# Optimization experiments

Hardware: AMD Instinct MI355X
Metric: run time of the kernel (lower is better)

Reference implementation:

```python
import jax, jax.numpy as jnp
import numpy as np


def setup_inputs() -> dict:
    key = jax.random.key(0)
    k1, k2 = jax.random.split(key)
    pred = jax.random.normal(k1, (1, 2048, 512), dtype=jnp.float32)
    cand = jax.random.normal(k2, (1, 65536, 512), dtype=jnp.float32)
    return {
        "predicted_transaction_company": pred,
        "future_transaction_companies_inc_current_data": cand,
    }


def reference(predicted_transaction_company, future_transaction_companies_inc_current_data):
    # torch.cdist with p=2 on [1,P,D] x [1,R,D] -> [1,P,R]; squeeze(0) -> [P,R]; global min.
    x = predicted_transaction_company[0]                       # [P, D]
    y = future_transaction_companies_inc_current_data[0]       # [R, D]
    sq = (
        jnp.sum(x * x, axis=-1)[:, None]
        + jnp.sum(y * y, axis=-1)[None, :]
        - 2.0 * jnp.einsum("pd,rd->pr", x, y)
    )                                                          # [P, R]
    distances = jnp.sqrt(jnp.maximum(sq, 0.0))
    return jnp.min(distances)
```

## Files before the change

### kernel.cpp

```cpp
#include <hip/hip_runtime.h>
#include <stdint.h>

#define P 2048
#define R 65536
#define DD 512
#define BT 128
#define BK 32

typedef __attribute__((ext_vector_type(8))) short short8;
typedef __attribute__((ext_vector_type(4))) float f32x4;

__device__ inline unsigned short f2bf(float f) {
  unsigned int u = __float_as_uint(f);
  u += 0x7fffu + ((u >> 16) & 1u);
  return (unsigned short)(u >> 16);
}

__device__ inline void gload_lds16(const void* g, void* l) {
  __builtin_amdgcn_global_load_lds(
      (const __attribute__((address_space(1))) unsigned int*)g,
      (__attribute__((address_space(3))) unsigned int*)l,
      16, 0, 0);
}

__global__ __launch_bounds__(256) void k_convert(
    const float* __restrict__ pred, const float* __restrict__ cand,
    unsigned short* __restrict__ Abf, unsigned short* __restrict__ Bbf,
    float* __restrict__ nx, float* __restrict__ ny,
    unsigned int* __restrict__ minp)
{
  if (blockIdx.x == 0 && threadIdx.x == 0) *minp = 0x7f800000u;
  int gw   = (blockIdx.x * 256 + threadIdx.x) >> 6;
  int lane = threadIdx.x & 63;
  if (gw >= P + R) return;
  const float* src; unsigned short* dst; float* np;
  if (gw < P) { src = pred + (size_t)gw * DD; dst = Abf + (size_t)gw * DD; np = nx + gw; }
  else { int r = gw - P; src = cand + (size_t)r * DD; dst = Bbf + (size_t)r * DD; np = ny + r; }
  const float4* s4 = ((const float4*)src) + lane * 2;
  float4 v0 = s4[0], v1 = s4[1];
  float ss = v0.x*v0.x + v0.y*v0.y + v0.z*v0.z + v0.w*v0.w
           + v1.x*v1.x + v1.y*v1.y + v1.z*v1.z + v1.w*v1.w;
  union { unsigned short h[8]; uint4 v; } pk;
  pk.h[0]=f2bf(v0.x); pk.h[1]=f2bf(v0.y); pk.h[2]=f2bf(v0.z); pk.h[3]=f2bf(v0.w);
  pk.h[4]=f2bf(v1.x); pk.h[5]=f2bf(v1.y); pk.h[6]=f2bf(v1.z); pk.h[7]=f2bf(v1.w);
  *(uint4*)(dst + (size_t)lane * 8) = pk.v;
  #pragma unroll
  for (int off = 32; off; off >>= 1) ss += __shfl_down(ss, off, 64);
  if (lane == 0) *np = ss;
}

__global__ __launch_bounds__(256) void k_gemm_min(
    const unsigned short* __restrict__ Abf, const unsigned short* __restrict__ Bbf,
    const float* __restrict__ nx, const float* __restrict__ ny,
    unsigned int* __restrict__ minp)
{
  __shared__ __align__(16) unsigned short As[BT * BK];
  __shared__ __align__(16) unsigned short Bs[BT * BK];
  __shared__ float wmin[4];

  const int tid  = threadIdx.x;
  const int wave = tid >> 6;
  const int lane = tid & 63;
  const int by = blockIdx.x & 15;
  const int bx = blockIdx.x >> 4;
  const int rowA0 = by * BT, rowB0 = bx * BT;
  const int wr = wave >> 1, wc = wave & 1;

  f32x4 zero = {0.f, 0.f, 0.f, 0.f};
  f32x4 acc[4][4];
  #pragma unroll
  for (int i = 0; i < 4; ++i)
    #pragma unroll
    for (int j = 0; j < 4; ++j) acc[i][j] = zero;

  const int t0 = wave * 2;
  const int r0 = t0 * 16 + (lane >> 2);
  const int cs = (lane & 3) * 8;
  const unsigned short* gA0 = Abf + (size_t)(rowA0 + r0) * DD + cs;
  const unsigned short* gA1 = Abf + (size_t)(rowA0 + r0 + 16) * DD + cs;
  const unsigned short* gB0 = Bbf + (size_t)(rowB0 + r0) * DD + cs;
  const unsigned short* gB1 = Bbf + (size_t)(rowB0 + r0 + 16) * DD + cs;
  unsigned short* lA0 = As + t0 * 512;
  unsigned short* lA1 = As + t0 * 512 + 512;
  unsigned short* lB0 = Bs + t0 * 512;
  unsigned short* lB1 = Bs + t0 * 512 + 512;

  const unsigned short* ap = As + ((wr * 64) + (lane & 15)) * BK + ((lane >> 4) * 8);
  const unsigned short* bp = Bs + ((wc * 64) + (lane & 15)) * BK + ((lane >> 4) * 8);

  for (int k0 = 0; k0 < DD; k0 += BK) {
    gload_lds16(gA0 + k0, lA0);
    gload_lds16(gA1 + k0, lA1);
    gload_lds16(gB0 + k0, lB0);
    gload_lds16(gB1 + k0, lB1);
    __syncthreads();

    short8 af[4], bfr[4];
    #pragma unroll
    for (int i = 0; i < 4; ++i) af[i]  = *(const short8*)(ap + i * 16 * BK);
    #pragma unroll
    for (int j = 0; j < 4; ++j) bfr[j] = *(const short8*)(bp + j * 16 * BK);
    #pragma unroll
    for (int i = 0; i < 4; ++i)
      #pragma unroll
      for (int j = 0; j < 4; ++j)
        acc[i][j] = __builtin_amdgcn_mfma_f32_16x16x32_bf16(af[i], bfr[j], acc[i][j], 0, 0, 0);
    __syncthreads();
  }

  const int quad = lane >> 4, n16 = lane & 15;
  float lmin = 3.4e38f;
  #pragma unroll
  for (int i = 0; i < 4; ++i) {
    const int mbase = rowA0 + wr * 64 + i * 16 + quad * 4;
    float4 nxv = *(const float4*)(nx + mbase);
    #pragma unroll
    for (int j = 0; j < 4; ++j) {
      const int n = rowB0 + wc * 64 + j * 16 + n16;
      const float nyv = ny[n];
      f32x4 a = acc[i][j];
      lmin = fminf(lmin, nxv.x + nyv - 2.0f * a[0]);
      lmin = fminf(lmin, nxv.y + nyv - 2.0f * a[1]);
      lmin = fminf(lmin, nxv.z + nyv - 2.0f * a[2]);
      lmin = fminf(lmin, nxv.w + nyv - 2.0f * a[3]);
    }
  }
  #pragma unroll
  for (int off = 32; off; off >>= 1) lmin = fminf(lmin, __shfl_down(lmin, off, 64));
  if (lane == 0) wmin[wave] = lmin;
  __syncthreads();
  if (tid == 0) {
    float m = fminf(fminf(wmin[0], wmin[1]), fminf(wmin[2], wmin[3]));
    atomicMin(minp, __float_as_uint(fmaxf(m, 0.0f)));
  }
}

__global__ __launch_bounds__(64) void k_initmin(unsigned int* minp) {
  if (threadIdx.x == 0) *minp = 0x7f800000u;
}

__global__ __launch_bounds__(256) void k_brute(
    const float* __restrict__ pred, const float* __restrict__ cand,
    unsigned int* __restrict__ minp)
{
  __shared__ float yrow[DD];
  __shared__ float wm[4];
  const int c = blockIdx.x;
  for (int i = threadIdx.x; i < DD; i += 256) yrow[i] = cand[(size_t)c * DD + i];
  __syncthreads();
  float lmin = 3.4e38f;
  for (int p = threadIdx.x; p < P; p += 256) {
    const float* xp = pred + (size_t)p * DD;
    float s = 0.f;
    for (int k = 0; k < DD; ++k) { float d = xp[k] - yrow[k]; s = fmaf(d, d, s); }
    lmin = fminf(lmin, s);
  }
  #pragma unroll
  for (int off = 32; off; off >>= 1) lmin = fminf(lmin, __shfl_down(lmin, off, 64));
  if ((threadIdx.x & 63) == 0) wm[threadIdx.x >> 6] = lmin;
  __syncthreads();
  if (threadIdx.x == 0) {
    float m = fminf(fminf(wm[0], wm[1]), fminf(wm[2], wm[3]));
    atomicMin(minp, __float_as_uint(fmaxf(m, 0.0f)));
  }
}

__global__ __launch_bounds__(64) void k_finalize(const unsigned int* minp, float* out) {
  if (threadIdx.x == 0) out[0] = sqrtf(__uint_as_float(*minp));
}

extern "C" void kernel_launch(void* const* d_in, const int* in_sizes, int n_in,
                              void* d_out, int out_size, void* d_ws, size_t ws_size,
                              hipStream_t stream) {
  const float* pred = (const float*)d_in[0];
  const float* cand = (const float*)d_in[1];
  float* out = (float*)d_out;

  unsigned int* minp = (unsigned int*)d_ws;
  float* wsf = (float*)d_ws;
  float* nx = wsf + 16;
  float* ny = nx + P;
  unsigned short* Abf = (unsigned short*)(ny + R);
  unsigned short* Bbf = Abf + (size_t)P * DD;
  const size_t need = (size_t)(16 + P + R) * 4 + ((size_t)P * DD + (size_t)R * DD) * 2;

  if (ws_size >= need) {
    const int rows = P + R;
    k_convert<<<rows / 4, 256, 0, stream>>>(pred, cand, Abf, Bbf, nx, ny, minp);
    k_gemm_min<<<(P / BT) * (R / BT), 256, 0, stream>>>(Abf, Bbf, nx, ny, minp);
  } else {
    k_initmin<<<1, 64, 0, stream>>>(minp);
    k_brute<<<R, 256, 0, stream>>>(pred, cand, minp);
  }
  k_finalize<<<1, 64, 0, stream>>>(minp, out);
}
```

Baseline: 402.6 us.

## Double K-tile depth to 64 and XOR-swizzle LDS layout for bank conflicts

Raises the K step of the bf16 MFMA GEMM tile from 32 to 64, so each barrier pair covers two MFMA rounds and the number of loop iterations and syncs is halved. The global-to-LDS loads are remapped to 8 rows per 16-byte-chunk group, with the column chunk XOR-swizzled by row, and the fragment reads apply the matching swizzle to avoid LDS bank conflicts on the 128-byte row stride. LDS use doubles to 32 KB per block, which may reduce occupancy, and there is still no double buffering.

```diff
diff --git a/kernel.cpp b/kernel.cpp
--- a/kernel.cpp
+++ b/kernel.cpp
@@ -5,7 +5,7 @@
 #define R 65536
 #define DD 512
 #define BT 128
-#define BK 32
+#define BK 64
 
 typedef __attribute__((ext_vector_type(8))) short short8;
 typedef __attribute__((ext_vector_type(4))) float f32x4;
@@ -73,33 +73,47 @@
     #pragma unroll
     for (int j = 0; j < 4; ++j) acc[i][j] = zero;
 
-  const int t0 = wave * 2;
-  const int r0 = t0 * 16 + (lane >> 2);
-  const int cs = (lane & 3) * 8;
-  const unsigned short* gA0 = Abf + (size_t)(rowA0 + r0) * DD + cs;
-  const unsigned short* gA1 = Abf + (size_t)(rowA0 + r0 + 16) * DD + cs;
-  const unsigned short* gB0 = Bbf + (size_t)(rowB0 + r0) * DD + cs;
-  const unsigned short* gB1 = Bbf + (size_t)(rowB0 + r0 + 16) * DD + cs;
-  unsigned short* lA0 = As + t0 * 512;
-  unsigned short* lA1 = As + t0 * 512 + 512;
-  unsigned short* lB0 = Bs + t0 * 512;
-  unsigned short* lB1 = Bs + t0 * 512 + 512;
-
-  const unsigned short* ap = As + ((wr * 64) + (lane & 15)) * BK + ((lane >> 4) * 8);
-  const unsigned short* bp = Bs + ((wc * 64) + (lane & 15)) * BK + ((lane >> 4) * 8);
+  const int rloc = lane >> 3;
+  const int cswz = (lane & 7) ^ rloc;
+  const unsigned short* gA[4]; const unsigned short* gB[4];
+  unsigned short* lA[4]; unsigned short* lB[4];
+  #pragma unroll
+  for (int t = 0; t < 4; ++t) {
+    const int rr = (wave * 4 + t) * 8 + rloc;
+    gA[t] = Abf + (size_t)(rowA0 + rr) * DD + cswz * 8;
+    gB[t] = Bbf + (size_t)(rowB0 + rr) * DD + cswz * 8;
+    lA[t] = As + (wave * 4 + t) * 512;
+    lB[t] = Bs + (wave * 4 + t) * 512;
+  }
+
+  const int m = lane & 15, quad = lane >> 4, mb = m & 7;
+  const unsigned short* apB = As + (wr * 64 + m) * BK;
+  const unsigned short* bpB = Bs + (wc * 64 + m) * BK;
+  const int sw0 = ((quad    ) ^ mb) * 8;
+  const int sw1 = ((quad + 4) ^ mb) * 8;
 
   for (int k0 = 0; k0 < DD; k0 += BK) {
-    gload_lds16(gA0 + k0, lA0);
-    gload_lds16(gA1 + k0, lA1);
-    gload_lds16(gB0 + k0, lB0);
-    gload_lds16(gB1 + k0, lB1);
+    #pragma unroll
+    for (int t = 0; t < 4; ++t) {
+      gload_lds16(gA[t] + k0, lA[t]);
+      gload_lds16(gB[t] + k0, lB[t]);
+    }
     __syncthreads();
 
     short8 af[4], bfr[4];
     #pragma unroll
-    for (int i = 0; i < 4; ++i) af[i]  = *(const short8*)(ap + i * 16 * BK);
-    #pragma unroll
-    for (int j = 0; j < 4; ++j) bfr[j] = *(const short8*)(bp + j * 16 * BK);
+    for (int i = 0; i < 4; ++i) af[i]  = *(const short8*)(apB + i * 16 * BK + sw0);
+    #pragma unroll
+    for (int j = 0; j < 4; ++j) bfr[j] = *(const short8*)(bpB + j * 16 * BK + sw0);
+    #pragma unroll
+    for (int i = 0; i < 4; ++i)
+      #pragma unroll
+      for (int j = 0; j < 4; ++j)
+        acc[i][j] = __builtin_amdgcn_mfma_f32_16x16x32_bf16(af[i], bfr[j], acc[i][j], 0, 0, 0);
+    #pragma unroll
+    for (int i = 0; i < 4; ++i) af[i]  = *(const short8*)(apB + i * 16 * BK + sw1);
+    #pragma unroll
+    for (int j = 0; j < 4; ++j) bfr[j] = *(const short8*)(bpB + j * 16 * BK + sw1);
     #pragma unroll
     for (int i = 0; i < 4; ++i)
       #pragma unroll
@@ -108,7 +122,7 @@
     __syncthreads();
   }
 
-  const int quad = lane >> 4, n16 = lane & 15;
+  const int n16 = lane & 15;
   float lmin = 3.4e38f;
   #pragma unroll
   for (int i = 0; i < 4; ++i) {
@@ -130,8 +144,8 @@
   if (lane == 0) wmin[wave] = lmin;
   __syncthreads();
   if (tid == 0) {
-    float m = fminf(fminf(wmin[0], wmin[1]), fminf(wmin[2], wmin[3]));
-    atomicMin(minp, __float_as_uint(fmaxf(m, 0.0f)));
+    float mn = fminf(fminf(wmin[0], wmin[1]), fminf(wmin[2], wmin[3]));
+    atomicMin(minp, __float_as_uint(fmaxf(mn, 0.0f)));
   }
 }
 
@@ -160,8 +174,8 @@
   if ((threadIdx.x & 63) == 0) wm[threadIdx.x >> 6] = lmin;
   __syncthreads();
   if (threadIdx.x == 0) {
-    float m = fminf(fminf(wm[0], wm[1]), fminf(wm[2], wm[3]));
-    atomicMin(minp, __float_as_uint(fmaxf(m, 0.0f)));
+    float mn = fminf(fminf(wm[0], wm[1]), fminf(wm[2], wm[3]));
+    atomicMin(minp, __float_as_uint(fmaxf(mn, 0.0f)));
   }
 }
 
```

Measured after the change: 398.5 us. About the same (-1.0%).

## Swizzle LDS layout, remap block order, fuse finalize via last-block counter

Applied to the files above, without the earlier changes.

Applies an XOR swizzle to the column chunk each lane loads into LDS and reads back for MFMA, aimed at removing LDS bank conflicts. Remaps block indices so groups of 8 adjacent B tiles share A tiles, for better L2 reuse. Drops the separate finalize kernel launch: a done counter lets the last block compute sqrt of the global min. The last-block pattern adds an atomic per block and relies on threadfence ordering.

```diff
diff --git a/kernel.cpp b/kernel.cpp
--- a/kernel.cpp
+++ b/kernel.cpp
@@ -6,6 +6,7 @@
 #define DD 512
 #define BT 128
 #define BK 32
+#define NBLK ((P / BT) * (R / BT))
 
 typedef __attribute__((ext_vector_type(8))) short short8;
 typedef __attribute__((ext_vector_type(4))) float f32x4;
@@ -27,9 +28,9 @@
     const float* __restrict__ pred, const float* __restrict__ cand,
     unsigned short* __restrict__ Abf, unsigned short* __restrict__ Bbf,
     float* __restrict__ nx, float* __restrict__ ny,
-    unsigned int* __restrict__ minp)
+    unsigned int* __restrict__ minp, unsigned int* __restrict__ done)
 {
-  if (blockIdx.x == 0 && threadIdx.x == 0) *minp = 0x7f800000u;
+  if (blockIdx.x == 0 && threadIdx.x == 0) { *minp = 0x7f800000u; *done = 0u; }
   int gw   = (blockIdx.x * 256 + threadIdx.x) >> 6;
   int lane = threadIdx.x & 63;
   if (gw >= P + R) return;
@@ -52,7 +53,8 @@
 __global__ __launch_bounds__(256) void k_gemm_min(
     const unsigned short* __restrict__ Abf, const unsigned short* __restrict__ Bbf,
     const float* __restrict__ nx, const float* __restrict__ ny,
-    unsigned int* __restrict__ minp)
+    unsigned int* __restrict__ minp, unsigned int* __restrict__ done,
+    float* __restrict__ out)
 {
   __shared__ __align__(16) unsigned short As[BT * BK];
   __shared__ __align__(16) unsigned short Bs[BT * BK];
@@ -61,8 +63,10 @@
   const int tid  = threadIdx.x;
   const int wave = tid >> 6;
   const int lane = tid & 63;
-  const int by = blockIdx.x & 15;
-  const int bx = blockIdx.x >> 4;
+
+  const int id = blockIdx.x;
+  const int by = (id >> 3) & 15;
+  const int bx = ((id >> 7) << 3) | (id & 7);
   const int rowA0 = by * BT, rowB0 = bx * BT;
   const int wr = wave >> 1, wc = wave & 1;
 
@@ -73,20 +77,22 @@
     #pragma unroll
     for (int j = 0; j < 4; ++j) acc[i][j] = zero;
 
-  const int t0 = wave * 2;
-  const int r0 = t0 * 16 + (lane >> 2);
-  const int cs = (lane & 3) * 8;
-  const unsigned short* gA0 = Abf + (size_t)(rowA0 + r0) * DD + cs;
-  const unsigned short* gA1 = Abf + (size_t)(rowA0 + r0 + 16) * DD + cs;
-  const unsigned short* gB0 = Bbf + (size_t)(rowB0 + r0) * DD + cs;
-  const unsigned short* gB1 = Bbf + (size_t)(rowB0 + r0 + 16) * DD + cs;
+  const int rloc = lane >> 2;
+  const int cswz = (lane & 3) ^ ((lane >> 3) & 3);
+  const int t0 = wave * 2, t1 = wave * 2 + 1;
+  const unsigned short* gA0 = Abf + (size_t)(rowA0 + 16 * t0 + rloc) * DD + cswz * 8;
+  const unsigned short* gA1 = Abf + (size_t)(rowA0 + 16 * t1 + rloc) * DD + cswz * 8;
+  const unsigned short* gB0 = Bbf + (size_t)(rowB0 + 16 * t0 + rloc) * DD + cswz * 8;
+  const unsigned short* gB1 = Bbf + (size_t)(rowB0 + 16 * t1 + rloc) * DD + cswz * 8;
   unsigned short* lA0 = As + t0 * 512;
-  unsigned short* lA1 = As + t0 * 512 + 512;
+  unsigned short* lA1 = As + t1 * 512;
   unsigned short* lB0 = Bs + t0 * 512;
-  unsigned short* lB1 = Bs + t0 * 512 + 512;
-
-  const unsigned short* ap = As + ((wr * 64) + (lane & 15)) * BK + ((lane >> 4) * 8);
-  const unsigned short* bp = Bs + ((wc * 64) + (lane & 15)) * BK + ((lane >> 4) * 8);
+  unsigned short* lB1 = Bs + t1 * 512;
+
+  const int m = lane & 15, quad = lane >> 4;
+  const int sw = (quad ^ ((m >> 1) & 3)) * 8;
+  const unsigned short* ap = As + (wr * 64 + m) * BK + sw;
+  const unsigned short* bp = Bs + (wc * 64 + m) * BK + sw;
 
   for (int k0 = 0; k0 < DD; k0 += BK) {
     gload_lds16(gA0 + k0, lA0);
@@ -108,7 +114,7 @@
     __syncthreads();
   }
 
-  const int quad = lane >> 4, n16 = lane & 15;
+  const int n16 = lane & 15;
   float lmin = 3.4e38f;
   #pragma unroll
   for (int i = 0; i < 4; ++i) {
@@ -130,8 +136,14 @@
   if (lane == 0) wmin[wave] = lmin;
   __syncthreads();
   if (tid == 0) {
-    float m = fminf(fminf(wmin[0], wmin[1]), fminf(wmin[2], wmin[3]));
-    atomicMin(minp, __float_as_uint(fmaxf(m, 0.0f)));
+    float mn = fminf(fminf(wmin[0], wmin[1]), fminf(wmin[2], wmin[3]));
+    atomicMin(minp, __float_as_uint(fmaxf(mn, 0.0f)));
+    __threadfence();
+    unsigned int old = atomicAdd(done, 1u);
+    if (old == (unsigned int)(NBLK - 1)) {
+      unsigned int bits = atomicMin(minp, 0x7f800000u);
+      out[0] = sqrtf(__uint_as_float(bits));
+    }
   }
 }
 
@@ -160,8 +172,8 @@
   if ((threadIdx.x & 63) == 0) wm[threadIdx.x >> 6] = lmin;
   __syncthreads();
   if (threadIdx.x == 0) {
-    float m = fminf(fminf(wm[0], wm[1]), fminf(wm[2], wm[3]));
-    atomicMin(minp, __float_as_uint(fmaxf(m, 0.0f)));
+    float mn = fminf(fminf(wm[0], wm[1]), fminf(wm[2], wm[3]));
+    atomicMin(minp, __float_as_uint(fmaxf(mn, 0.0f)));
   }
 }
 
@@ -177,20 +189,21 @@
   float* out = (float*)d_out;
 
   unsigned int* minp = (unsigned int*)d_ws;
+  unsigned int* done = ((unsigned int*)d_ws) + 32;
   float* wsf = (float*)d_ws;
-  float* nx = wsf + 16;
+  float* nx = wsf + 64;
   float* ny = nx + P;
   unsigned short* Abf = (unsigned short*)(ny + R);
   unsigned short* Bbf = Abf + (size_t)P * DD;
-  const size_t need = (size_t)(16 + P + R) * 4 + ((size_t)P * DD + (size_t)R * DD) * 2;
+  const size_t need = (size_t)(64 + P + R) * 4 + ((size_t)P * DD + (size_t)R * DD) * 2;
 
   if (ws_size >= need) {
     const int rows = P + R;
-    k_convert<<<rows / 4, 256, 0, stream>>>(pred, cand, Abf, Bbf, nx, ny, minp);
-    k_gemm_min<<<(P / BT) * (R / BT), 256, 0, stream>>>(Abf, Bbf, nx, ny, minp);
+    k_convert<<<rows / 4, 256, 0, stream>>>(pred, cand, Abf, Bbf, nx, ny, minp, done);
+    k_gemm_min<<<NBLK, 256, 0, stream>>>(Abf, Bbf, nx, ny, minp, done, out);
   } else {
     k_initmin<<<1, 64, 0, stream>>>(minp);
     k_brute<<<R, 256, 0, stream>>>(pred, cand, minp);
-  }
-  k_finalize<<<1, 64, 0, stream>>>(minp, out);
-}
+    k_finalize<<<1, 64, 0, stream>>>(minp, out);
+  }
+}
```

After: 488.8 us. +21.4%, slower.
